# Optimization experiments

Hardware: AMD Instinct MI355X
Metric: run time of the kernel (lower is better)

The kernel has to match this reference:

```python
import jax, jax.numpy as jnp
import numpy as np
import math

B, H, W = 8, 512, 1024
BOUNDARY_WIDTH = 4
BOUNDARY_ITERATION = 4
KERNEL_SIZE = 7
DILATION_SIZE = 6
NEG = -1e30  # geodesic border for morphological dilation (kornia border_type='geodesic')
POS = 1e30   # geodesic border for erosion
DN = ('NCHW', 'OIHW', 'NCHW')


def _gaussian_kernel():
    size, sigma = 7, 1.0
    g = np.fromfunction(
        lambda x, y: 1.0 / (2 * math.pi * sigma ** 2)
        * math.e ** (-(((x - (size - 1) / 2) ** 2 + (y - (size - 1) / 2) ** 2) / (2 * sigma ** 2))),
        (size, size))
    g = g / g.sum()
    return jnp.asarray(g, jnp.float32)[None, None]  # [1,1,7,7]


def _cross_dilate(x):
    # morphological dilation with 3x3 cross structuring element (generate_binary_structure(2,1))
    p = jnp.pad(x, ((0, 0), (0, 0), (1, 1), (1, 1)), constant_values=NEG)
    c = p[..., 1:-1, 1:-1]
    return jnp.maximum(
        jnp.maximum(jnp.maximum(c, p[..., :-2, 1:-1]), p[..., 2:, 1:-1]),
        jnp.maximum(p[..., 1:-1, :-2], p[..., 1:-1, 2:]))


def _erode3(x):
    # morphological erosion with full 3x3 ones structuring element, geodesic border
    return jax.lax.reduce_window(x, jnp.float32(POS), jax.lax.min,
                                 (1, 1, 3, 3), (1, 1, 1, 1),
                                 [(0, 0), (0, 0), (1, 1), (1, 1)])


def _conv3_sum(x):
    # 3x3 all-ones conv (first_conv), VALID on already-padded input
    k = jnp.ones((1, 1, 3, 3), x.dtype)
    return jax.lax.conv_general_dilated(x, k, (1, 1), 'VALID', dimension_numbers=DN)


def _forward(x, prediction):
    lab = prediction.astype(jnp.float32)
    # boundaries where dilated labels differ from eroded labels
    boundaries = (_cross_dilate(lab) != _erode3(lab)).astype(jnp.float32)
    out = x
    diff = BOUNDARY_WIDTH // BOUNDARY_ITERATION
    for it in range(BOUNDARY_ITERATION):
        prev = out
        r = 0 if (BOUNDARY_WIDTH == 0 or it == BOUNDARY_ITERATION - 1) else BOUNDARY_WIDTH - diff * it - 1
        eb = boundaries
        for _ in range(r):  # dilation by diamond of radius r == r cross-dilations
            eb = _cross_dilate(eb)
        mask = (eb == 0).astype(jnp.float32)  # non-boundary mask
        xm = out * mask
        xp = jnp.pad(xm, ((0, 0), (0, 0), (1, 1), (1, 1)), mode='edge')       # ReplicationPad2d(1)
        mp = jnp.pad(mask, ((0, 0), (0, 0), (1, 1), (1, 1)), mode='edge')
        y = _conv3_sum(xp)
        n = _conv3_sum(mp).astype(jnp.int32)  # .long() truncation; values are exact small ints
        n_safe = jnp.where(n == 0, 1, n).astype(y.dtype)
        avg = jnp.where(n == 0, prev, y / n_safe)
        out = jnp.where(mask == 0, avg, prev)
    # dilated gaussian smoothing: ReplicationPad2d(18) + 7x7 conv, dilation 6
    pad = DILATION_SIZE * 3
    op = jnp.pad(out, ((0, 0), (0, 0), (pad, pad), (pad, pad)), mode='edge')
    out = jax.lax.conv_general_dilated(op, _gaussian_kernel(), (1, 1), 'VALID',
                                       rhs_dilation=(DILATION_SIZE, DILATION_SIZE),
                                       dimension_numbers=DN)
    return out


def setup_inputs() -> dict:
    key = jax.random.key(0)
    k1, k2 = jax.random.split(key)
    x = jax.random.normal(k1, (B, 1, H, W), dtype=jnp.float32)
    prediction = jax.random.randint(k2, (B, 1, H, W), 0, 19, dtype=jnp.int32)
    return {"x": x, "prediction": prediction}


def reference(x, prediction):
    return _forward(x, prediction)
```

## Files before the change

### kernel.cpp

```cpp
#include <hip/hip_runtime.h>

#define B_ 8
#define H_ 512
#define W_ 1024
#define NPX (B_*H_*W_)

#define TILE 32
#define HD 4
#define RD 40
#define HB 7
#define RB 46
#define HP 8
#define RP 48
#define TP 36

__device__ __forceinline__ int clampi(int v, int lo, int hi) {
    return v < lo ? lo : (v > hi ? hi : v);
}
__device__ __forceinline__ int imax(int a, int b) { return a > b ? a : b; }
__device__ __forceinline__ int imin(int a, int b) { return a < b ? a : b; }

__global__ __launch_bounds__(256)
void k_stage1(const float* __restrict__ xg, const int* __restrict__ predg,
              float* __restrict__ midg, unsigned char* __restrict__ flags)
{
    __shared__ int sScratch[3200];
    __shared__ unsigned long long sB[4][RB];
    __shared__ float sA[RD * RD];
    __shared__ float sC[RD * RD];
    __shared__ int sV[4];

    int*   sPred = sScratch;
    float* sHX = (float*)sScratch;
    float* sHM = (float*)sScratch + RD * RD;

    const int tid = threadIdx.x;
    const int x0 = blockIdx.x * TILE;
    const int y0 = blockIdx.y * TILE;
    const size_t plane = (size_t)H_ * W_;
    const int*   pp = predg + blockIdx.z * plane;
    const float* xp = xg    + blockIdx.z * plane;
    float*       op = midg  + blockIdx.z * plane;

    for (int i = tid; i < TP * TP; i += 256) {
        int ry = i / TP, rx = i - ry * TP;
        int gy = y0 - 2 + ry, gx = x0 - 2 + rx;
        sPred[i] = (gy >= 0 && gy < H_ && gx >= 0 && gx < W_) ? pp[(size_t)gy * W_ + gx] : -1;
    }
    __syncthreads();

    const int lane = tid & 63, wv = tid >> 6;
    unsigned long long acc = 0ULL;
    for (int r = wv; r < TILE + 2; r += 4) {
        bool viol = false;
        if (lane < TILE + 2) {
            int gy = y0 - 1 + r, gx = x0 - 1 + lane;
            if (gy >= 0 && gy < H_ && gx >= 0 && gx < W_) {
                const int py = r + 1, px = lane + 1;
                int c  = sPred[py * TP + px];
                int up = sPred[(py - 1) * TP + px];
                int dn = sPred[(py + 1) * TP + px];
                int lf = sPred[py * TP + px - 1];
                int rt = sPred[py * TP + px + 1];
                int ul = sPred[(py - 1) * TP + px - 1];
                int ur = sPred[(py - 1) * TP + px + 1];
                int dl = sPred[(py + 1) * TP + px - 1];
                int dr = sPred[(py + 1) * TP + px + 1];
                int mx = imax(imax(up, dn), imax(lf, rt));
                int Bv = 0x7fffffff;
                int mn = imin(imin(imin(up < 0 ? Bv : up, dn < 0 ? Bv : dn),
                                   imin(lf < 0 ? Bv : lf, rt < 0 ? Bv : rt)),
                              imin(imin(ul < 0 ? Bv : ul, ur < 0 ? Bv : ur),
                                   imin(dl < 0 ? Bv : dl, dr < 0 ? Bv : dr)));
                viol = !((mx > c) || (mn < c));
            }
        }
        acc |= __ballot(viol);
    }
    if (lane == 0) sV[wv] = (acc != 0ULL) ? 1 : 0;
    __syncthreads();
    const bool dirty = (sV[0] | sV[1] | sV[2] | sV[3]) != 0;

    const int tileId = (((blockIdx.z << 4) + blockIdx.y) << 5) + blockIdx.x;
    if (!dirty) {
        if (flags) {
            if (tid == 0) flags[tileId] = 0;
        } else {
            int ty = tid >> 3, tx4 = (tid & 7) * 4;
            const float4 v = *(const float4*)(xp + (size_t)(y0 + ty) * W_ + (x0 + tx4));
            *(float4*)(op + (size_t)(y0 + ty) * W_ + (x0 + tx4)) = v;
        }
        return;
    }

    const bool leftB  = (x0 == 0), rightB = (x0 + TILE == W_);
    const bool topB   = (y0 == 0), botB   = (y0 + TILE == H_);
    const bool borderB = leftB || rightB || topB || botB;

    __syncthreads();
    for (int i = tid; i < RP * RP; i += 256) {
        int ry = i / RP, rx = i - ry * RP;
        int gy = y0 - HP + ry, gx = x0 - HP + rx;
        sPred[i] = (gy >= 0 && gy < H_ && gx >= 0 && gx < W_) ? pp[(size_t)gy * W_ + gx] : -1;
    }
    for (int i = tid; i < RD * RD; i += 256) {
        int ry = i / RD, rx = i - ry * RD;
        int gy = clampi(y0 - HD + ry, 0, H_ - 1);
        int gx = clampi(x0 - HD + rx, 0, W_ - 1);
        sA[i] = xp[(size_t)gy * W_ + gx];
    }
    __syncthreads();

    {
        for (int row = wv; row < RB; row += 4) {
            bool bp = false;
            if (lane < RB) {
                const int py = row + 1, px = lane + 1;
                int c = sPred[py * RP + px];
                if (c >= 0) {
                    int up = sPred[(py - 1) * RP + px];
                    int dn = sPred[(py + 1) * RP + px];
                    int lf = sPred[py * RP + px - 1];
                    int rt = sPred[py * RP + px + 1];
                    int ul = sPred[(py - 1) * RP + px - 1];
                    int ur = sPred[(py - 1) * RP + px + 1];
                    int dl = sPred[(py + 1) * RP + px - 1];
                    int dr = sPred[(py + 1) * RP + px + 1];
                    int mx = imax(imax(up, dn), imax(lf, rt));
                    int Bv = 0x7fffffff;
                    int mn = imin(imin(imin(up < 0 ? Bv : up, dn < 0 ? Bv : dn),
                                       imin(lf < 0 ? Bv : lf, rt < 0 ? Bv : rt)),
                                  imin(imin(ul < 0 ? Bv : ul, ur < 0 ? Bv : ur),
                                       imin(dl < 0 ? Bv : dl, dr < 0 ? Bv : dr)));
                    bp = (mx > c) || (mn < c);
                }
            }
            unsigned long long bal = __ballot(bp);
            if (lane == 0) sB[0][row] = bal;
        }
    }

    #pragma unroll
    for (int lvl = 1; lvl < 4; ++lvl) {
        __syncthreads();
        if (tid < RB) {
            unsigned long long c = sB[lvl - 1][tid];
            unsigned long long u = (tid > 0)      ? sB[lvl - 1][tid - 1] : 0ULL;
            unsigned long long d = (tid < RB - 1) ? sB[lvl - 1][tid + 1] : 0ULL;
            sB[lvl][tid] = c | (c << 1) | (c >> 1) | u | d;
        }
    }
    __syncthreads();

    if (borderB) {
        const bool act = tid < 4 * RB;
        unsigned long long val = 0; int lvl = 0, row = 0;
        if (act) {
            lvl = tid / RB; row = tid - lvl * RB;
            int srcRow = clampi(row, topB ? HB : 0, botB ? (RB - 1 - HB) : RB - 1);
            val = sB[lvl][srcRow];
            if (leftB) {
                unsigned long long b = (val >> HB) & 1ULL;
                unsigned long long lo = (1ULL << HB) - 1;
                val = (val & ~lo) | (b ? lo : 0ULL);
            }
            if (rightB) {
                const int jb = RB - 1 - HB;
                unsigned long long b = (val >> jb) & 1ULL;
                unsigned long long keep = (1ULL << (jb + 1)) - 1;
                unsigned long long hi = (((1ULL << RB) - 1) & ~keep);
                val = (val & keep) | (b ? hi : 0ULL);
            }
        }
        __syncthreads();
        if (act) sB[lvl][row] = val;
    }
    __syncthreads();

    float* cur = sA;
    float* nxt = sC;
    #pragma unroll
    for (int it = 0; it < 4; ++it) {
        const int r = 3 - it;
        const unsigned long long* br = sB[r];

        for (int i = tid; i < RD * RD; i += 256) {
            int ry = i / RD, rx = i - ry * RD;
            unsigned long long row = br[ry + (HB - HD)];
            int rxm = rx > 0 ? rx - 1 : 0;
            int rxp = rx < RD - 1 ? rx + 1 : RD - 1;
            float m0 = ((row >> (rx + 2)) & 1ULL) ? 0.f : 1.f;
            float m1 = ((row >> (rx + 3)) & 1ULL) ? 0.f : 1.f;
            float m2 = ((row >> (rx + 4)) & 1ULL) ? 0.f : 1.f;
            float a0 = cur[ry * RD + rxm];
            float a1 = cur[ry * RD + rx];
            float a2 = cur[ry * RD + rxp];
            sHX[i] = m0 * a0 + m1 * a1 + m2 * a2;
            sHM[i] = m0 + m1 + m2;
        }
        __syncthreads();

        for (int i = tid; i < 38 * 38; i += 256) {
            int q = i / 38;
            int ry = 1 + q, rx = 1 + (i - q * 38);
            int idx = ry * RD + rx;
            float n = sHM[idx - RD] + sHM[idx] + sHM[idx + RD];
            float y = sHX[idx - RD] + sHX[idx] + sHX[idx + RD];
            float c = cur[idx];
            unsigned long long row = br[ry + (HB - HD)];
            bool masked = ((row >> (rx + 3)) & 1ULL) != 0ULL;
            float avg = y * __builtin_amdgcn_rcpf(n);
            nxt[idx] = (masked && n > 0.5f) ? avg : c;
        }
        __syncthreads();

        if (borderB) {
            for (int i = tid; i < RD * RD; i += 256) {
                int ry = i / RD, rx = i - ry * RD;
                int ryc = clampi(ry, topB ? HD : 0, botB ? (RD - 1 - HD) : RD - 1);
                int rxc = clampi(rx, leftB ? HD : 0, rightB ? (RD - 1 - HD) : RD - 1);
                if (ryc != ry || rxc != rx) nxt[i] = nxt[ryc * RD + rxc];
            }
        }
        __syncthreads();
        float* t = cur; cur = nxt; nxt = t;
    }

    for (int i = tid; i < TILE * TILE; i += 256) {
        int ty = i >> 5, tx = i & 31;
        op[(size_t)(y0 + ty) * W_ + (x0 + tx)] = cur[(ty + HD) * RD + (tx + HD)];
    }
    if (flags && tid == 0) flags[tileId] = 1;
}

#define GW0 0.39905027965f
#define GW1 0.24203622800f
#define GW2 0.05400558260f
#define GW3 0.00443304810f

__global__ __launch_bounds__(256)
void gaussH(const float* __restrict__ x, const float* __restrict__ mid,
            const unsigned char* __restrict__ flags, float* __restrict__ out)
{
    __shared__ int sDirty;
    const int tid = threadIdx.x;
    const int grow = blockIdx.x;
    const int img = grow >> 9, y = grow & (H_ - 1);
    const int fbase = (((img << 4) + (y >> 5)) << 5);

    if (tid == 0) sDirty = 0;
    __syncthreads();
    if (tid < 64) {
        int f = (tid < 32) ? (int)flags[fbase + tid] : 0;
        bool any = __any(f != 0);
        if (tid == 0 && any) sDirty = 1;
    }
    __syncthreads();

    const float* rp = x   + (size_t)grow * W_;
    float*       wp = out + (size_t)grow * W_;
    const int gx0 = tid * 4;
    float4 o;

    if (!sDirty) {
        if (tid >= 5 && tid <= 250) {
            const float4* vp = (const float4*)(rp + gx0 - 20);
            float4 fm5 = vp[0], fm4 = vp[1], fm3 = vp[2], fm2 = vp[3], fm1 = vp[4];
            float4 f0 = vp[5], f1 = vp[6], f2 = vp[7], f3 = vp[8], f4 = vp[9], f5 = vp[10];
            o.x = GW0 * f0.x + GW1 * (fm2.z + f1.z) + GW2 * (fm3.x + f3.x) + GW3 * (fm5.z + f4.z);
            o.y = GW0 * f0.y + GW1 * (fm2.w + f1.w) + GW2 * (fm3.y + f3.y) + GW3 * (fm5.w + f4.w);
            o.z = GW0 * f0.z + GW1 * (fm1.x + f2.x) + GW2 * (fm3.z + f3.z) + GW3 * (fm4.x + f5.x);
            o.w = GW0 * f0.w + GW1 * (fm1.y + f2.y) + GW2 * (fm3.w + f3.w) + GW3 * (fm4.y + f5.y);
        } else {
            float r[4];
            #pragma unroll
            for (int j = 0; j < 4; ++j) {
                int gx = gx0 + j;
                r[j] = GW3 * (rp[clampi(gx - 18, 0, W_ - 1)] + rp[clampi(gx + 18, 0, W_ - 1)])
                     + GW2 * (rp[clampi(gx - 12, 0, W_ - 1)] + rp[clampi(gx + 12, 0, W_ - 1)])
                     + GW1 * (rp[clampi(gx - 6,  0, W_ - 1)] + rp[clampi(gx + 6,  0, W_ - 1)])
                     + GW0 *  rp[gx];
            }
            o.x = r[0]; o.y = r[1]; o.z = r[2]; o.w = r[3];
        }
    } else {
        const float* rm = mid + (size_t)grow * W_;
        float r[4];
        #pragma unroll
        for (int j = 0; j < 4; ++j) {
            int gx = gx0 + j;
            float t[7];
            #pragma unroll
            for (int k = 0; k < 7; ++k) {
                int q = clampi(gx + (k - 3) * 6, 0, W_ - 1);
                t[k] = flags[fbase + (q >> 5)] ? rm[q] : rp[q];
            }
            r[j] = GW3 * (t[0] + t[6]) + GW2 * (t[1] + t[5]) + GW1 * (t[2] + t[4]) + GW0 * t[3];
        }
        o.x = r[0]; o.y = r[1]; o.z = r[2]; o.w = r[3];
    }
    *(float4*)(wp + gx0) = o;
}

__global__ __launch_bounds__(256)
void gaussV(const float* __restrict__ in, float* __restrict__ out)
{
    const int tid = threadIdx.x;
    const int y   = blockIdx.x & (H_ - 1);
    const int img = blockIdx.x >> 9;
    const float* pl = in  + (size_t)img * H_ * W_;
    float*       wp = out + (size_t)blockIdx.x * W_;
    const int gx0 = tid * 4;

    const float* r0 = pl + (size_t)clampi(y - 18, 0, H_ - 1) * W_ + gx0;
    const float* r1 = pl + (size_t)clampi(y - 12, 0, H_ - 1) * W_ + gx0;
    const float* r2 = pl + (size_t)clampi(y - 6,  0, H_ - 1) * W_ + gx0;
    const float* r3 = pl + (size_t)y * W_ + gx0;
    const float* r4 = pl + (size_t)clampi(y + 6,  0, H_ - 1) * W_ + gx0;
    const float* r5 = pl + (size_t)clampi(y + 12, 0, H_ - 1) * W_ + gx0;
    const float* r6 = pl + (size_t)clampi(y + 18, 0, H_ - 1) * W_ + gx0;

    float4 a0 = *(const float4*)r0, a1 = *(const float4*)r1, a2 = *(const float4*)r2;
    float4 a3 = *(const float4*)r3, a4 = *(const float4*)r4, a5 = *(const float4*)r5;
    float4 a6 = *(const float4*)r6;

    float4 o;
    o.x = GW3 * (a0.x + a6.x) + GW2 * (a1.x + a5.x) + GW1 * (a2.x + a4.x) + GW0 * a3.x;
    o.y = GW3 * (a0.y + a6.y) + GW2 * (a1.y + a5.y) + GW1 * (a2.y + a4.y) + GW0 * a3.y;
    o.z = GW3 * (a0.z + a6.z) + GW2 * (a1.z + a5.z) + GW1 * (a2.z + a4.z) + GW0 * a3.z;
    o.w = GW3 * (a0.w + a6.w) + GW2 * (a1.w + a5.w) + GW1 * (a2.w + a4.w) + GW0 * a3.w;
    *(float4*)(wp + gx0) = o;
}

#define GTW 64
#define GTH 64
#define GHALO 18
#define GRH (GTH + 2*GHALO)

__global__ __launch_bounds__(256)
void bsws_stage2_tiled(const float* __restrict__ ing, float* __restrict__ outg)
{
    __shared__ float sH[GRH][GTW];
    const int tid = threadIdx.x;
    const int x0 = blockIdx.x * GTW;
    const int y0 = blockIdx.y * GTH;
    const size_t plane = (size_t)H_ * W_;
    const float* ip = ing  + blockIdx.z * plane;
    float*       op = outg + blockIdx.z * plane;

    for (int i = tid; i < GRH * GTW; i += 256) {
        int row = i >> 6, col = i & 63;
        int gy = clampi(y0 - GHALO + row, 0, H_ - 1);
        const float* rowp = ip + (size_t)gy * W_;
        int gx = x0 + col;
        float acc = GW3 * (rowp[clampi(gx - 18, 0, W_ - 1)] + rowp[clampi(gx + 18, 0, W_ - 1)])
                  + GW2 * (rowp[clampi(gx - 12, 0, W_ - 1)] + rowp[clampi(gx + 12, 0, W_ - 1)])
                  + GW1 * (rowp[clampi(gx - 6,  0, W_ - 1)] + rowp[clampi(gx + 6,  0, W_ - 1)])
                  + GW0 *  rowp[gx];
        sH[row][col] = acc;
    }
    __syncthreads();
    for (int i = tid; i < GTH * GTW; i += 256) {
        int ty = i >> 6, tx = i & 63;
        float acc = GW3 * (sH[ty][tx]      + sH[ty + 36][tx])
                  + GW2 * (sH[ty + 6][tx]  + sH[ty + 30][tx])
                  + GW1 * (sH[ty + 12][tx] + sH[ty + 24][tx])
                  + GW0 *  sH[ty + 18][tx];
        op[(size_t)(y0 + ty) * W_ + (x0 + tx)] = acc;
    }
}

extern "C" void kernel_launch(void* const* d_in, const int* in_sizes, int n_in,
                              void* d_out, int out_size, void* d_ws, size_t ws_size,
                              hipStream_t stream) {
    const float* x    = (const float*)d_in[0];
    const int*   pred = (const int*)d_in[1];
    float*       out  = (float*)d_out;
    float*       mid  = (float*)d_ws;

    const size_t plane_bytes = (size_t)NPX * 4;
    const dim3 g1(W_ / TILE, H_ / TILE, B_);

    if (ws_size >= 2 * plane_bytes + 4096) {
        float* midH = mid + NPX;
        unsigned char* flags = (unsigned char*)d_ws + 2 * plane_bytes;
        k_stage1<<<g1, 256, 0, stream>>>(x, pred, mid, flags);
        gaussH<<<B_ * H_, 256, 0, stream>>>(x, mid, flags, midH);
        gaussV<<<B_ * H_, 256, 0, stream>>>(midH, out);
    } else {
        k_stage1<<<g1, 256, 0, stream>>>(x, pred, mid, nullptr);
        bsws_stage2_tiled<<<dim3(W_ / GTW, H_ / GTH, B_), dim3(256), 0, stream>>>(mid, out);
    }
}
```

Measured before the change: 129.0 us.

## Fuse separable Gaussian passes into one tiled kernel and vectorize label halo load

Replaces the separate horizontal and vertical Gaussian kernels, which went through a full-plane intermediate buffer, with one tiled kernel. It computes the horizontal pass for a 128x64 tile plus an 18-row halo into shared memory, then runs the vertical pass from there. The dirty-flag check now covers every stage-1 tile the halo touches. The stage-1 label halo load is widened to 40 columns so interior tiles can use int4 loads. This removes one kernel launch and a global write and read of an intermediate plane, at the cost of recomputing the halo rows and using more shared memory per block.

```diff
diff --git a/kernel.cpp b/kernel.cpp
--- a/kernel.cpp
+++ b/kernel.cpp
@@ -12,7 +12,6 @@
 #define RB 46
 #define HP 8
 #define RP 48
-#define TP 36
 
 __device__ __forceinline__ int clampi(int v, int lo, int hi) {
     return v < lo ? lo : (v > hi ? hi : v);
@@ -42,10 +41,22 @@
     const float* xp = xg    + blockIdx.z * plane;
     float*       op = midg  + blockIdx.z * plane;
 
-    for (int i = tid; i < TP * TP; i += 256) {
-        int ry = i / TP, rx = i - ry * TP;
-        int gy = y0 - 2 + ry, gx = x0 - 2 + rx;
-        sPred[i] = (gy >= 0 && gy < H_ && gx >= 0 && gx < W_) ? pp[(size_t)gy * W_ + gx] : -1;
+    const bool leftB  = (x0 == 0), rightB = (x0 + TILE == W_);
+    const bool topB   = (y0 == 0), botB   = (y0 + TILE == H_);
+    const bool borderB = leftB || rightB || topB || botB;
+
+    if (!borderB) {
+        for (int i = tid; i < 36 * 10; i += 256) {
+            int ry = i / 10, c4 = i - ry * 10;
+            int4 v = *(const int4*)(pp + (size_t)(y0 - 2 + ry) * W_ + (x0 - 4) + 4 * c4);
+            *(int4*)&sPred[ry * 40 + 4 * c4] = v;
+        }
+    } else {
+        for (int i = tid; i < 36 * 40; i += 256) {
+            int ry = i / 40, c = i - ry * 40;
+            int gy = y0 - 2 + ry, gx = x0 - 4 + c;
+            sPred[i] = (gy >= 0 && gy < H_ && gx >= 0 && gx < W_) ? pp[(size_t)gy * W_ + gx] : -1;
+        }
     }
     __syncthreads();
 
@@ -56,16 +67,16 @@
         if (lane < TILE + 2) {
             int gy = y0 - 1 + r, gx = x0 - 1 + lane;
             if (gy >= 0 && gy < H_ && gx >= 0 && gx < W_) {
-                const int py = r + 1, px = lane + 1;
-                int c  = sPred[py * TP + px];
-                int up = sPred[(py - 1) * TP + px];
-                int dn = sPred[(py + 1) * TP + px];
-                int lf = sPred[py * TP + px - 1];
-                int rt = sPred[py * TP + px + 1];
-                int ul = sPred[(py - 1) * TP + px - 1];
-                int ur = sPred[(py - 1) * TP + px + 1];
-                int dl = sPred[(py + 1) * TP + px - 1];
-                int dr = sPred[(py + 1) * TP + px + 1];
+                const int py = r + 1, px = lane + 3;
+                int c  = sPred[py * 40 + px];
+                int up = sPred[(py - 1) * 40 + px];
+                int dn = sPred[(py + 1) * 40 + px];
+                int lf = sPred[py * 40 + px - 1];
+                int rt = sPred[py * 40 + px + 1];
+                int ul = sPred[(py - 1) * 40 + px - 1];
+                int ur = sPred[(py - 1) * 40 + px + 1];
+                int dl = sPred[(py + 1) * 40 + px - 1];
+                int dr = sPred[(py + 1) * 40 + px + 1];
                 int mx = imax(imax(up, dn), imax(lf, rt));
                 int Bv = 0x7fffffff;
                 int mn = imin(imin(imin(up < 0 ? Bv : up, dn < 0 ? Bv : dn),
@@ -92,10 +103,6 @@
         }
         return;
     }
-
-    const bool leftB  = (x0 == 0), rightB = (x0 + TILE == W_);
-    const bool topB   = (y0 == 0), botB   = (y0 + TILE == H_);
-    const bool borderB = leftB || rightB || topB || botB;
 
     __syncthreads();
     for (int i = tid; i < RP * RP; i += 256) {
@@ -239,97 +246,113 @@
 #define GW3 0.00443304810f
 
 __global__ __launch_bounds__(256)
-void gaussH(const float* __restrict__ x, const float* __restrict__ mid,
-            const unsigned char* __restrict__ flags, float* __restrict__ out)
+void gaussF(const float* __restrict__ xg, const float* __restrict__ midg,
+            const unsigned char* __restrict__ flags, float* __restrict__ outg)
 {
+    __shared__ float sH[100][128];
     __shared__ int sDirty;
+
     const int tid = threadIdx.x;
-    const int grow = blockIdx.x;
-    const int img = grow >> 9, y = grow & (H_ - 1);
-    const int fbase = (((img << 4) + (y >> 5)) << 5);
+    const int x0 = blockIdx.x * 128;
+    const int y0 = blockIdx.y * 64;
+    const int img = blockIdx.z;
+    const size_t plane = (size_t)H_ * W_;
+    const float* xp = xg  + (size_t)img * plane;
+    float*       op = outg + (size_t)img * plane;
 
     if (tid == 0) sDirty = 0;
     __syncthreads();
-    if (tid < 64) {
-        int f = (tid < 32) ? (int)flags[fbase + tid] : 0;
-        bool any = __any(f != 0);
-        if (tid == 0 && any) sDirty = 1;
-    }
-    __syncthreads();
-
-    const float* rp = x   + (size_t)grow * W_;
-    float*       wp = out + (size_t)grow * W_;
-    const int gx0 = tid * 4;
-    float4 o;
+    {
+        const int tyLo = ((y0 >= 18) ? y0 - 18 : 0) >> 5;
+        const int tyHi = ((y0 + 81 < H_) ? y0 + 81 : H_ - 1) >> 5;
+        const int txLo = ((x0 >= 18) ? x0 - 18 : 0) >> 5;
+        const int txHi = ((x0 + 145 < W_) ? x0 + 145 : W_ - 1) >> 5;
+        const int ntx = txHi - txLo + 1;
+        const int n = (tyHi - tyLo + 1) * ntx;
+        if (tid < 64) {
+            bool d = false;
+            if (tid < n) {
+                int q = tid / ntx;
+                int ty = tyLo + q, tx = txLo + (tid - q * ntx);
+                d = flags[(((img << 4) + ty) << 5) + tx] != 0;
+            }
+            unsigned long long bal = __ballot(d);
+            if (tid == 0 && bal != 0ULL) sDirty = 1;
+        }
+    }
+    __syncthreads();
 
     if (!sDirty) {
-        if (tid >= 5 && tid <= 250) {
-            const float4* vp = (const float4*)(rp + gx0 - 20);
-            float4 fm5 = vp[0], fm4 = vp[1], fm3 = vp[2], fm2 = vp[3], fm1 = vp[4];
-            float4 f0 = vp[5], f1 = vp[6], f2 = vp[7], f3 = vp[8], f4 = vp[9], f5 = vp[10];
-            o.x = GW0 * f0.x + GW1 * (fm2.z + f1.z) + GW2 * (fm3.x + f3.x) + GW3 * (fm5.z + f4.z);
-            o.y = GW0 * f0.y + GW1 * (fm2.w + f1.w) + GW2 * (fm3.y + f3.y) + GW3 * (fm5.w + f4.w);
-            o.z = GW0 * f0.z + GW1 * (fm1.x + f2.x) + GW2 * (fm3.z + f3.z) + GW3 * (fm4.x + f5.x);
-            o.w = GW0 * f0.w + GW1 * (fm1.y + f2.y) + GW2 * (fm3.w + f3.w) + GW3 * (fm4.y + f5.y);
-        } else {
-            float r[4];
+        for (int i = tid; i < 100 * 32; i += 256) {
+            int row = i >> 5, cg = i & 31;
+            int gx0 = x0 + cg * 4;
+            int gy = clampi(y0 - 18 + row, 0, H_ - 1);
+            const float* rp = xp + (size_t)gy * W_;
+            float4 o;
+            if (gx0 >= 20 && gx0 <= 1000) {
+                const float4* vp = (const float4*)(rp + gx0 - 20);
+                float4 fm5 = vp[0], fm4 = vp[1], fm3 = vp[2], fm2 = vp[3], fm1 = vp[4];
+                float4 f0 = vp[5], f1 = vp[6], f2 = vp[7], f3 = vp[8], f4 = vp[9], f5 = vp[10];
+                o.x = GW0 * f0.x + GW1 * (fm2.z + f1.z) + GW2 * (fm3.x + f3.x) + GW3 * (fm5.z + f4.z);
+                o.y = GW0 * f0.y + GW1 * (fm2.w + f1.w) + GW2 * (fm3.y + f3.y) + GW3 * (fm5.w + f4.w);
+                o.z = GW0 * f0.z + GW1 * (fm1.x + f2.x) + GW2 * (fm3.z + f3.z) + GW3 * (fm4.x + f5.x);
+                o.w = GW0 * f0.w + GW1 * (fm1.y + f2.y) + GW2 * (fm3.w + f3.w) + GW3 * (fm4.y + f5.y);
+            } else {
+                float r4[4];
+                #pragma unroll
+                for (int j = 0; j < 4; ++j) {
+                    int gx = gx0 + j;
+                    r4[j] = GW3 * (rp[clampi(gx - 18, 0, W_ - 1)] + rp[clampi(gx + 18, 0, W_ - 1)])
+                          + GW2 * (rp[clampi(gx - 12, 0, W_ - 1)] + rp[clampi(gx + 12, 0, W_ - 1)])
+                          + GW1 * (rp[clampi(gx - 6,  0, W_ - 1)] + rp[clampi(gx + 6,  0, W_ - 1)])
+                          + GW0 *  rp[gx];
+                }
+                o.x = r4[0]; o.y = r4[1]; o.z = r4[2]; o.w = r4[3];
+            }
+            *(float4*)&sH[row][cg * 4] = o;
+        }
+    } else {
+        const float* mp = midg + (size_t)img * plane;
+        for (int i = tid; i < 100 * 32; i += 256) {
+            int row = i >> 5, cg = i & 31;
+            int gy = clampi(y0 - 18 + row, 0, H_ - 1);
+            const float* rx = xp + (size_t)gy * W_;
+            const float* rm = mp + (size_t)gy * W_;
+            const int frow = ((img << 4) + (gy >> 5)) << 5;
+            float r4[4];
             #pragma unroll
             for (int j = 0; j < 4; ++j) {
-                int gx = gx0 + j;
-                r[j] = GW3 * (rp[clampi(gx - 18, 0, W_ - 1)] + rp[clampi(gx + 18, 0, W_ - 1)])
-                     + GW2 * (rp[clampi(gx - 12, 0, W_ - 1)] + rp[clampi(gx + 12, 0, W_ - 1)])
-                     + GW1 * (rp[clampi(gx - 6,  0, W_ - 1)] + rp[clampi(gx + 6,  0, W_ - 1)])
-                     + GW0 *  rp[gx];
-            }
-            o.x = r[0]; o.y = r[1]; o.z = r[2]; o.w = r[3];
-        }
-    } else {
-        const float* rm = mid + (size_t)grow * W_;
-        float r[4];
-        #pragma unroll
-        for (int j = 0; j < 4; ++j) {
-            int gx = gx0 + j;
-            float t[7];
-            #pragma unroll
-            for (int k = 0; k < 7; ++k) {
-                int q = clampi(gx + (k - 3) * 6, 0, W_ - 1);
-                t[k] = flags[fbase + (q >> 5)] ? rm[q] : rp[q];
-            }
-            r[j] = GW3 * (t[0] + t[6]) + GW2 * (t[1] + t[5]) + GW1 * (t[2] + t[4]) + GW0 * t[3];
-        }
-        o.x = r[0]; o.y = r[1]; o.z = r[2]; o.w = r[3];
-    }
-    *(float4*)(wp + gx0) = o;
-}
-
-__global__ __launch_bounds__(256)
-void gaussV(const float* __restrict__ in, float* __restrict__ out)
-{
-    const int tid = threadIdx.x;
-    const int y   = blockIdx.x & (H_ - 1);
-    const int img = blockIdx.x >> 9;
-    const float* pl = in  + (size_t)img * H_ * W_;
-    float*       wp = out + (size_t)blockIdx.x * W_;
-    const int gx0 = tid * 4;
-
-    const float* r0 = pl + (size_t)clampi(y - 18, 0, H_ - 1) * W_ + gx0;
-    const float* r1 = pl + (size_t)clampi(y - 12, 0, H_ - 1) * W_ + gx0;
-    const float* r2 = pl + (size_t)clampi(y - 6,  0, H_ - 1) * W_ + gx0;
-    const float* r3 = pl + (size_t)y * W_ + gx0;
-    const float* r4 = pl + (size_t)clampi(y + 6,  0, H_ - 1) * W_ + gx0;
-    const float* r5 = pl + (size_t)clampi(y + 12, 0, H_ - 1) * W_ + gx0;
-    const float* r6 = pl + (size_t)clampi(y + 18, 0, H_ - 1) * W_ + gx0;
-
-    float4 a0 = *(const float4*)r0, a1 = *(const float4*)r1, a2 = *(const float4*)r2;
-    float4 a3 = *(const float4*)r3, a4 = *(const float4*)r4, a5 = *(const float4*)r5;
-    float4 a6 = *(const float4*)r6;
-
-    float4 o;
-    o.x = GW3 * (a0.x + a6.x) + GW2 * (a1.x + a5.x) + GW1 * (a2.x + a4.x) + GW0 * a3.x;
-    o.y = GW3 * (a0.y + a6.y) + GW2 * (a1.y + a5.y) + GW1 * (a2.y + a4.y) + GW0 * a3.y;
-    o.z = GW3 * (a0.z + a6.z) + GW2 * (a1.z + a5.z) + GW1 * (a2.z + a4.z) + GW0 * a3.z;
-    o.w = GW3 * (a0.w + a6.w) + GW2 * (a1.w + a5.w) + GW1 * (a2.w + a4.w) + GW0 * a3.w;
-    *(float4*)(wp + gx0) = o;
+                int gx = x0 + cg * 4 + j;
+                float t[7];
+                #pragma unroll
+                for (int k = 0; k < 7; ++k) {
+                    int q = clampi(gx + (k - 3) * 6, 0, W_ - 1);
+                    t[k] = flags[frow + (q >> 5)] ? rm[q] : rx[q];
+                }
+                r4[j] = GW3 * (t[0] + t[6]) + GW2 * (t[1] + t[5]) + GW1 * (t[2] + t[4]) + GW0 * t[3];
+            }
+            float4 o; o.x = r4[0]; o.y = r4[1]; o.z = r4[2]; o.w = r4[3];
+            *(float4*)&sH[row][cg * 4] = o;
+        }
+    }
+    __syncthreads();
+
+    for (int i = tid; i < 64 * 32; i += 256) {
+        int r = i >> 5, cg = i & 31;
+        float4 a0 = *(const float4*)&sH[r][cg * 4];
+        float4 a1 = *(const float4*)&sH[r + 6][cg * 4];
+        float4 a2 = *(const float4*)&sH[r + 12][cg * 4];
+        float4 a3 = *(const float4*)&sH[r + 18][cg * 4];
+        float4 a4 = *(const float4*)&sH[r + 24][cg * 4];
+        float4 a5 = *(const float4*)&sH[r + 30][cg * 4];
+        float4 a6 = *(const float4*)&sH[r + 36][cg * 4];
+        float4 o;
+        o.x = GW3 * (a0.x + a6.x) + GW2 * (a1.x + a5.x) + GW1 * (a2.x + a4.x) + GW0 * a3.x;
+        o.y = GW3 * (a0.y + a6.y) + GW2 * (a1.y + a5.y) + GW1 * (a2.y + a4.y) + GW0 * a3.y;
+        o.z = GW3 * (a0.z + a6.z) + GW2 * (a1.z + a5.z) + GW1 * (a2.z + a4.z) + GW0 * a3.z;
+        o.w = GW3 * (a0.w + a6.w) + GW2 * (a1.w + a5.w) + GW1 * (a2.w + a4.w) + GW0 * a3.w;
+        *(float4*)(op + (size_t)(y0 + r) * W_ + (x0 + cg * 4)) = o;
+    }
 }
 
 #define GTW 64
@@ -340,7 +363,7 @@
 __global__ __launch_bounds__(256)
 void bsws_stage2_tiled(const float* __restrict__ ing, float* __restrict__ outg)
 {
-    __shared__ float sH[GRH][GTW];
+    __shared__ float sHt[GRH][GTW];
     const int tid = threadIdx.x;
     const int x0 = blockIdx.x * GTW;
     const int y0 = blockIdx.y * GTH;
@@ -357,15 +380,15 @@
                   + GW2 * (rowp[clampi(gx - 12, 0, W_ - 1)] + rowp[clampi(gx + 12, 0, W_ - 1)])
                   + GW1 * (rowp[clampi(gx - 6,  0, W_ - 1)] + rowp[clampi(gx + 6,  0, W_ - 1)])
                   + GW0 *  rowp[gx];
-        sH[row][col] = acc;
+        sHt[row][col] = acc;
     }
     __syncthreads();
     for (int i = tid; i < GTH * GTW; i += 256) {
         int ty = i >> 6, tx = i & 63;
-        float acc = GW3 * (sH[ty][tx]      + sH[ty + 36][tx])
-                  + GW2 * (sH[ty + 6][tx]  + sH[ty + 30][tx])
-                  + GW1 * (sH[ty + 12][tx] + sH[ty + 24][tx])
-                  + GW0 *  sH[ty + 18][tx];
+        float acc = GW3 * (sHt[ty][tx]      + sHt[ty + 36][tx])
+                  + GW2 * (sHt[ty + 6][tx]  + sHt[ty + 30][tx])
+                  + GW1 * (sHt[ty + 12][tx] + sHt[ty + 24][tx])
+                  + GW0 *  sHt[ty + 18][tx];
         op[(size_t)(y0 + ty) * W_ + (x0 + tx)] = acc;
     }
 }
@@ -381,12 +404,10 @@
     const size_t plane_bytes = (size_t)NPX * 4;
     const dim3 g1(W_ / TILE, H_ / TILE, B_);
 
-    if (ws_size >= 2 * plane_bytes + 4096) {
-        float* midH = mid + NPX;
-        unsigned char* flags = (unsigned char*)d_ws + 2 * plane_bytes;
+    if (ws_size >= plane_bytes + 4096) {
+        unsigned char* flags = (unsigned char*)d_ws + plane_bytes;
         k_stage1<<<g1, 256, 0, stream>>>(x, pred, mid, flags);
-        gaussH<<<B_ * H_, 256, 0, stream>>>(x, mid, flags, midH);
-        gaussV<<<B_ * H_, 256, 0, stream>>>(midH, out);
+        gaussF<<<dim3(W_ / 128, H_ / 64, B_), 256, 0, stream>>>(x, mid, flags, out);
     } else {
         k_stage1<<<g1, 256, 0, stream>>>(x, pred, mid, nullptr);
         bsws_stage2_tiled<<<dim3(W_ / GTW, H_ / GTH, B_), dim3(256), 0, stream>>>(mid, out);
```

Measured after the change: 149.5 us. 15.9% more time.
